# Performance work log

Measured on AMD Instinct MI355X. Metric: run time of the kernel, lower is better.

The kernel has to match this reference:

```python
import jax, jax.numpy as jnp
from jax import lax
import numpy as np

NBINS = 50

def _make_filters():
    coords = np.linspace(-1.0, 1.0, 3)
    zz, yy, xx = np.meshgrid(coords, coords, coords, indexing='ij')
    gf = []
    for freq in [2.0, 4.0]:
        for ang in [0.0, np.pi / 4, np.pi / 2, 3 * np.pi / 4]:
            gauss = np.exp(-(xx ** 2 + yy ** 2 + zz ** 2) / 0.5)
            f = gauss * np.cos(freq * (xx * np.cos(ang) + yy * np.sin(ang)))
            f = f - f.mean()
            s = f.std(ddof=1)  # torch std is unbiased
            if s > 1e-8:
                f = f / s
            gf.append(f)
    gf = np.stack(gf)[:, None].astype(np.float32)  # (8,1,3,3,3)
    lf = []
    for axis in range(3):
        for sign in [1, -1]:
            f = np.zeros((3, 3, 3), np.float32)
            f[1, 1, 1] = 1.0
            idx = [1, 1, 1]
            idx[axis] += sign
            f[tuple(idx)] = -1.0
            lf.append(f)
    lf = np.stack(lf)[:, None].astype(np.float32)  # (6,1,3,3,3)
    return gf, lf

def setup_inputs() -> dict:
    key = jax.random.key(0)
    k1, k2 = jax.random.split(key)
    B, D, H, W = 4, 96, 160, 160
    x = jax.random.uniform(k1, (B, 1, D, H, W), jnp.float32, minval=-1.0, maxval=1.0)
    mask = (jax.random.uniform(k2, (B, 1, D, H, W), jnp.float32) > 0.5).astype(jnp.float32)
    gf, lf = _make_filters()
    return {"x": x, "mask": mask, "gabor_filters": jnp.asarray(gf), "lbp_filters": jnp.asarray(lf)}

def _hu_stats(v, mf):
    # v, mf: (B,D,H,W); mf is 0/1 float mask
    n = mf.sum((1, 2, 3))                      # (B,)
    nn = jnp.maximum(n, 1.0)
    mu = (mf * v).sum((1, 2, 3)) / nn
    diff = (v - mu[:, None, None, None]) * mf
    var = (diff ** 2).sum((1, 2, 3)) / jnp.maximum(n - 1.0, 1.0)  # unbiased, like torch .std()
    sigma = jnp.sqrt(var) + 1e-8
    z = diff / sigma[:, None, None, None]
    skew = (z ** 3).sum((1, 2, 3)) / nn
    kurt = (z ** 4).sum((1, 2, 3)) / nn - 3.0
    # histogram over [-1,1] with 50 bins; torch.histc ignores out-of-range, last bin inclusive
    w = mf * ((v >= -1.0) & (v <= 1.0)).astype(v.dtype)
    idx = jnp.clip(jnp.floor((v + 1.0) * (NBINS / 2.0)).astype(jnp.int32), 0, NBINS - 1)
    hist = jax.vmap(lambda i, wb: jnp.zeros((NBINS,), v.dtype).at[i.ravel()].add(wb.ravel()))(idx, w)
    p = hist / (hist.sum(-1, keepdims=True) + 1e-8)
    ent = -(p * jnp.log(p + 1e-8)).sum(-1)
    valid = (n >= 10.0).astype(v.dtype)
    return jnp.stack([mu, sigma, skew, kurt, ent], axis=1) * valid[:, None]  # (B,5)

def _glcm_proxy(v, m):
    # v: (B,D,H,W) float; m: (B,D,H,W) bool
    rows = []
    for axis in range(3):
        a = axis + 1
        sl1 = tuple(slice(None, -1) if i == a else slice(None) for i in range(4))
        sl2 = tuple(slice(1, None) if i == a else slice(None) for i in range(4))
        d = v[sl1] - v[sl2]
        mp = (m[sl1] & m[sl2]).astype(v.dtype)
        s = mp.sum((1, 2, 3))
        ss = jnp.maximum(s, 1.0)
        con = (mp * d * d).sum((1, 2, 3)) / ss
        hom = (mp / (1.0 + d * d)).sum((1, 2, 3)) / ss
        ok = (s >= 4.0).astype(v.dtype)
        rows += [con * ok, hom * ok]
    return jnp.stack(rows, axis=1)  # (B,6)

def _forward(x, mask, gabor_filters, lbp_filters):
    v = x[:, 0]                       # (B,D,H,W)
    m = mask[:, 0] > 0.5              # bool
    mf = m.astype(x.dtype)
    hu = _hu_stats(v, mf)             # (B,5)
    dn = ('NCDHW', 'OIDHW', 'NCDHW')
    pad = [(1, 1)] * 3
    gab = lax.conv_general_dilated(x, gabor_filters, (1, 1, 1), pad, dimension_numbers=dn)
    lung_vol = jnp.clip(mask.sum((2, 3, 4)), 1.0, None)      # (B,1)
    gab_feat = jnp.abs(gab * mask).sum((2, 3, 4)) / lung_vol  # (B,8)
    lbp = lax.conv_general_dilated(x, lbp_filters, (1, 1, 1), pad, dimension_numbers=dn)
    lbp = lbp * mask
    lbp_feat = ((lbp > 0).astype(x.dtype) * mask).sum((2, 3, 4)) / lung_vol  # (B,6)
    glcm = _glcm_proxy(v, m)          # (B,6)
    return jnp.concatenate([hu, gab_feat, lbp_feat, glcm], axis=1)  # (B,25)

def reference(x, mask, gabor_filters, lbp_filters):
    return _forward(x, mask, gabor_filters, lbp_filters)
```

## Files before the change

kernel.cpp:

```cpp
#include <hip/hip_runtime.h>
#include <math.h>

#define B_    4
#define D_    96
#define H_    160
#define W_    160
#define HW_   (H_ * W_)
#define NVOX  (D_ * H_ * W_)
#define NBINS 50
#define CZ    8
#define NCHUNK (D_ / CZ)
#define NTILE 50
#define NSLOTS (NTILE * NCHUNK)
#define NITEMS (B_ * NSLOTS)
#define NQR   28
#define PART_F (B_ * NQR * NSLOTS)
#define HIST_U PART_F
#define WQ_F   (PART_F + 200)
#define CTR_U  (WQ_F + 40)
#define LASTP ((D_ - 1) * HW_)

typedef float f2 __attribute__((ext_vector_type(2)));

__device__ __forceinline__ float rfl(float v) {
    return __uint_as_float(__builtin_amdgcn_readfirstlane(__float_as_uint(v)));
}

__global__ __launch_bounds__(64) void radiomics_weights(
    const float* __restrict__ gf, const float* __restrict__ lf,
    float* __restrict__ ws)
{
    const int lane = threadIdx.x;
    __shared__ float sCs[8][5], sR[8], sMO[8], sMC[8];
    if (lane < 8) {
        const int f = lane;
        float O9[9], C9[9];
        float mC = 0.f, mO = 0.f;
#pragma unroll
        for (int k = 0; k < 9; ++k) {
            O9[k] = gf[f * 27 + k];
            C9[k] = gf[f * 27 + 9 + k];
            mC += C9[k]; mO += O9[k];
        }
        mC *= (1.f / 9.f); mO *= (1.f / 9.f);
        float cov = 0.f, var = 0.f;
#pragma unroll
        for (int k = 0; k < 9; ++k) {
            float c = C9[k] - mC, o = O9[k] - mO;
            cov += c * o; var += c * c;
        }
        sR[f] = cov / var; sMO[f] = mO; sMC[f] = mC;
#pragma unroll
        for (int j = 0; j < 4; ++j) sCs[f][j] = 0.5f * (C9[j] + C9[8 - j]);
        sCs[f][4] = C9[4];
    }
    __syncthreads();
    if (lane == 0) {
        float* wq = ws + WQ_F;
        float gz0 = 0.f;
        for (int f = 0; f < 8; ++f) gz0 += sR[f];
        gz0 *= 0.125f;
        wq[0] = gz0;
        float df[8];
        for (int f = 0; f < 8; ++f) df[f] = sMO[f] - gz0 * sMC[f];
        for (int F = 0; F < 2; ++F) {
            const int f0 = 4 * F, f1 = 4 * F + 1, f2 = 4 * F + 2, f3 = 4 * F + 3;
            float* g = wq + 1 + 11 * F;
            g[0]  = 0.5f * (df[f0] + df[f2]);
            g[1]  = 0.5f * (sCs[f0][0] + sCs[f2][0]);
            g[2]  = 0.5f * (sCs[f0][2] + sCs[f2][2]);
            g[3]  = 0.5f * (sCs[f0][4] + sCs[f2][4]);
            g[4]  = 0.5f * (sCs[f0][1] + sCs[f2][3]);
            g[5]  = 0.5f * (sCs[f0][3] + sCs[f2][1]);
            g[6]  = 0.5f * (df[f1] + df[f3]);
            g[7]  = 0.25f * (sCs[f1][1] + sCs[f1][3]
                           + sCs[f3][1] + sCs[f3][3]);
            g[8]  = 0.5f * (sCs[f1][4] + sCs[f3][4]);
            g[9]  = 0.5f * (sCs[f1][0] + sCs[f3][2]);
            g[10] = 0.5f * (sCs[f1][2] + sCs[f3][0]);
        }
        const int nbidx[6] = {22, 4, 16, 10, 14, 12};
        for (int f = 0; f < 6; ++f) {
            wq[23 + f] = lf[f * 27 + 13];
            wq[29 + f] = lf[f * 27 + nbidx[f]];
        }
        ((unsigned int*)ws)[CTR_U] = 0u;
    }
    unsigned int* gh = (unsigned int*)ws + HIST_U;
    for (int i = lane; i < B_ * NBINS; i += 64) gh[i] = 0u;
}

#define LOADP(s, zo) do {                                                   \
    _Pragma("unroll")                                                       \
    for (int r_ = 0; r_ < 3; ++r_) {                                        \
        Xw[s][r_][0] = xbb[(zo) + rowoff[r_] + xL];                         \
        f2 t_ = *(const f2*)(xbb + (zo) + rowoff[r_] + gx);                 \
        Xw[s][r_][1] = t_.x; Xw[s][r_][2] = t_.y;                           \
        Xw[s][r_][3] = xbb[(zo) + rowoff[r_] + xR];                         \
    }                                                                       \
} while (0)

#define FINISH(s, bzv) do {                                                 \
    const float br0_ = bndRow0 * (bzv), br2_ = bndRow2 * (bzv);             \
    _Pragma("unroll")                                                       \
    for (int c_ = 0; c_ < 4; ++c_) {                                        \
        Xw[s][0][c_] *= br0_; Xw[s][2][c_] *= br2_; Xw[s][1][c_] *= (bzv);  \
    }                                                                       \
    _Pragma("unroll")                                                       \
    for (int r_ = 0; r_ < 3; ++r_) {                                        \
        Xw[s][r_][0] *= bndL; Xw[s][r_][3] *= bndR;                         \
    }                                                                       \
    {                                                                       \
        float cs0_ = Xw[s][0][0] + Xw[s][1][0] + Xw[s][2][0];               \
        float cs1_ = Xw[s][0][1] + Xw[s][1][1] + Xw[s][2][1];               \
        float cs2_ = Xw[s][0][2] + Xw[s][1][2] + Xw[s][2][2];               \
        float cs3_ = Xw[s][0][3] + Xw[s][1][3] + Xw[s][2][3];               \
        S9[s][0] = cs0_ + cs1_ + cs2_;                                      \
        S9[s][1] = cs1_ + cs2_ + cs3_;                                      \
    }                                                                       \
} while (0)

__global__ __launch_bounds__(256) void radiomics_main(
    const float* __restrict__ x, const float* __restrict__ mask,
    float* __restrict__ ws)
{
    __shared__ unsigned int shist[4 * NBINS];
    __shared__ float xred[4][NQR];
    __shared__ unsigned int sitem;

    const int tid = threadIdx.x;
    const int tx = tid & 15, ty = tid >> 4;
    const int lane = tid & 63, wid = tid >> 6;

    const float* wq = ws + WQ_F;
    const float gz0 = rfl(wq[0]);
    float gco[22];
#pragma unroll
    for (int i = 0; i < 22; ++i) gco[i] = rfl(wq[1 + i]);
    float lwc[6], lwn[6];
#pragma unroll
    for (int f = 0; f < 6; ++f) { lwc[f] = rfl(wq[23 + f]); lwn[f] = rfl(wq[29 + f]); }

    unsigned int* ctr   = (unsigned int*)ws + CTR_U;
    unsigned int* ghist = (unsigned int*)ws + HIST_U;

    for (;;) {
        __syncthreads();
        if (tid == 0) sitem = atomicAdd(ctr, 1u);
        for (int i = tid; i < 4 * NBINS; i += 256) shist[i] = 0u;
        __syncthreads();
        const int item = __builtin_amdgcn_readfirstlane((int)sitem);
        if (item >= NITEMS) break;

        const int b   = item / NSLOTS;
        const int s   = item - b * NSLOTS;
        const int cz  = s / NTILE;
        const int bix = s - cz * NTILE;
        const int z0  = cz * CZ;
        const int gx = (bix % 5) * 32 + tx * 2;
        const int gy = (bix / 5) * 16 + ty;

        const float* __restrict__ xbb = x    + (size_t)b * NVOX;
        const float* __restrict__ mbb = mask + (size_t)b * NVOX;

        const int gy0 = (gy > 0) ? gy - 1 : 0;
        const int gy2 = (gy + 1 < H_) ? gy + 1 : H_ - 1;
        const int rowoff[3] = { gy0 * W_, gy * W_, gy2 * W_ };
        const float bndRow0 = (gy > 0) ? 1.f : 0.f;
        const float bndRow2 = (gy + 1 < H_) ? 1.f : 0.f;
        const int xL = (gx > 0) ? gx - 1 : 0;
        const int xR = (gx + 2 < W_) ? gx + 2 : W_ - 1;
        const float bndL = (gx > 0) ? 1.f : 0.f;
        const float bndR = (gx + 2 < W_) ? 1.f : 0.f;
        const int moff  = gy * W_ + gx;
        const int myoff = gy2 * W_ + gx;
        const int mxoff = gy * W_ + xR;
        const float bym = bndRow2, bxm = bndR;

        float Xw[4][3][4];
        float S9[4][2];
        float Mq[4][2];
        float bzs[4];
        f2    myq[2];
        float mxq[2];
        float acc[NQR];
#pragma unroll
        for (int q = 0; q < NQR; ++q) acc[q] = 0.f;
        bzs[0] = bzs[1] = bzs[2] = 1.f;

        if (z0 == 0) {
#pragma unroll
            for (int r = 0; r < 3; ++r)
#pragma unroll
                for (int c = 0; c < 4; ++c) Xw[0][r][c] = 0.f;
            S9[0][0] = S9[0][1] = 0.f;
        } else {
            LOADP(0, (z0 - 1) * HW_);
            FINISH(0, 1.f);
        }
        LOADP(1, z0 * HW_);
        FINISH(1, 1.f);
        {
            f2 mm = *(const f2*)(mbb + z0 * HW_ + moff);
            Mq[1][0] = (mm.x > 0.5f) ? 1.f : 0.f;
            Mq[1][1] = (mm.y > 0.5f) ? 1.f : 0.f;
        }
        LOADP(2, (z0 + 1) * HW_);
        {
            f2 mm = *(const f2*)(mbb + (z0 + 1) * HW_ + moff);
            Mq[2][0] = mm.x; Mq[2][1] = mm.y;
        }
        Mq[0][0] = Mq[0][1] = 0.f;
        myq[0] = *(const f2*)(mbb + z0 * HW_ + myoff);
        mxq[0] = mbb[z0 * HW_ + mxoff];

        int zc   = z0 * HW_;
        int zpre = (z0 + 2) * HW_;

#pragma unroll 1
        for (int i0 = 0; i0 < CZ; i0 += 4) {
#pragma unroll
            for (int j = 0; j < 4; ++j) {
                const int c0 = j, c1 = (j + 1) & 3, c2 = (j + 2) & 3, c3 = (j + 3) & 3;
                const int cur = j & 1, nxt = cur ^ 1;

                const int zpe = (zpre < NVOX) ? zpre : LASTP;
                bzs[c3] = (zpre < NVOX) ? 1.f : 0.f;
                LOADP(c3, zpe);
                {
                    f2 mm = *(const f2*)(mbb + zpe + moff);
                    Mq[c3][0] = mm.x; Mq[c3][1] = mm.y;
                }
                const int zn = (zc + HW_ < NVOX) ? zc + HW_ : LASTP;
                myq[nxt] = *(const f2*)(mbb + zn + myoff);
                mxq[nxt] = mbb[zn + mxoff];

                FINISH(c2, bzs[c2]);
                Mq[c2][0] = (Mq[c2][0] * bzs[c2] > 0.5f) ? 1.f : 0.f;
                Mq[c2][1] = (Mq[c2][1] * bzs[c2] > 0.5f) ? 1.f : 0.f;

                float T6[3][4];
#pragma unroll
                for (int r = 0; r < 3; ++r)
#pragma unroll
                    for (int c = 0; c < 4; ++c)
                        T6[r][c] = fmaf(gz0, Xw[c0][r][c] + Xw[c2][r][c], Xw[c1][r][c]);

                const f2 my2 = myq[cur];
                const float mxs = mxq[cur];

#pragma unroll
                for (int q = 0; q < 2; ++q) {
                    const float v  = Xw[c1][1][q + 1];
                    const float mc = Mq[c1][q];

                    acc[0] += mc;
                    float mv  = mc * v;  acc[1] += mv;
                    float mv2 = mv * v;  acc[2] += mv2;
                    float mv3 = mv2 * v; acc[3] += mv3;
                    acc[4] += mv3 * v;

                    if (mc > 0.5f && v >= -1.f && v <= 1.f) {
                        int bi = (int)floorf((v + 1.f) * (NBINS * 0.5f));
                        bi = min(max(bi, 0), NBINS - 1);
                        atomicAdd(&shist[(tid >> 6) * NBINS + bi], 1u);
                    }

                    float P0 = T6[0][q]     + T6[2][q + 2];
                    float P1 = T6[0][q + 1] + T6[2][q + 1];
                    float P2 = T6[0][q + 2] + T6[2][q];
                    float P3 = T6[1][q]     + T6[1][q + 2];
                    float ctrv = T6[1][q + 1];
                    float S2 = S9[c0][q] + S9[c2][q];
                    float Qv = P1 + P3;
#pragma unroll
                    for (int F = 0; F < 2; ++F) {
                        const float dfA = gco[F*11+0], c0s = gco[F*11+1];
                        const float c2s = gco[F*11+2], c4s = gco[F*11+3];
                        const float cu  = gco[F*11+4], cw  = gco[F*11+5];
                        const float dfB = gco[F*11+6], ct  = gco[F*11+7];
                        const float ce  = gco[F*11+8], ca  = gco[F*11+9];
                        const float cb  = gco[F*11+10];
                        float E = dfA * S2;
                        E = fmaf(c0s, P0, E); E = fmaf(c2s, P2, E); E = fmaf(c4s, ctrv, E);
                        float r0   = fmaf(cu, P1, fmaf(cw, P3, E));
                        float r90  = fmaf(cw, P1, fmaf(cu, P3, E));
                        float G = fmaf(ct, Qv, dfB * S2);
                        G = fmaf(ce, ctrv, G);
                        float r45  = fmaf(ca, P0, fmaf(cb, P2, G));
                        float r135 = fmaf(cb, P0, fmaf(ca, P2, G));
                        acc[5 + 4*F + 0] = fmaf(fabsf(r0),   mc, acc[5 + 4*F + 0]);
                        acc[5 + 4*F + 1] = fmaf(fabsf(r45),  mc, acc[5 + 4*F + 1]);
                        acc[5 + 4*F + 2] = fmaf(fabsf(r90),  mc, acc[5 + 4*F + 2]);
                        acc[5 + 4*F + 3] = fmaf(fabsf(r135), mc, acc[5 + 4*F + 3]);
                    }

                    const float nb[6] = { Xw[c2][1][q + 1], Xw[c0][1][q + 1],
                                          Xw[c1][2][q + 1], Xw[c1][0][q + 1],
                                          Xw[c1][1][q + 2], Xw[c1][1][q] };
#pragma unroll
                    for (int f = 0; f < 6; ++f) {
                        float l = fmaf(lwc[f], v, lwn[f] * nb[f]);
                        acc[13 + f] += (l > 0.f) ? mc : 0.f;
                    }

                    {
                        float mp = mc * Mq[c2][q];
                        float d = v - Xw[c2][1][q + 1], dd = d * d;
                        acc[19] += mp;
                        acc[22] = fmaf(mp, dd, acc[22]);
                        acc[25] = fmaf(mp, __builtin_amdgcn_rcpf(1.f + dd), acc[25]);
                    }
                    {
                        float mr = (q == 0) ? my2.x : my2.y;
                        float mp = mc * (((mr > 0.5f) ? 1.f : 0.f) * bym);
                        float d = v - Xw[c1][2][q + 1], dd = d * d;
                        acc[20] += mp;
                        acc[23] = fmaf(mp, dd, acc[23]);
                        acc[26] = fmaf(mp, __builtin_amdgcn_rcpf(1.f + dd), acc[26]);
                    }
                    {
                        float mnr = (q == 0) ? Mq[c1][1] : (((mxs > 0.5f) ? 1.f : 0.f) * bxm);
                        float mp = mc * mnr;
                        float d = v - Xw[c1][1][q + 2], dd = d * d;
                        acc[21] += mp;
                        acc[24] = fmaf(mp, dd, acc[24]);
                        acc[27] = fmaf(mp, __builtin_amdgcn_rcpf(1.f + dd), acc[27]);
                    }
                }
                zc += HW_; zpre += HW_;
            }
        }

#pragma unroll
        for (int q = 0; q < NQR; ++q) {
            float sm = acc[q];
#pragma unroll
            for (int o = 32; o > 0; o >>= 1)
                sm += __shfl_down(sm, o, 64);
            acc[q] = sm;
        }
        if (lane == 0) {
#pragma unroll
            for (int q = 0; q < NQR; ++q) xred[wid][q] = acc[q];
        }
        __syncthreads();

        if (tid < NQR) {
            float v = xred[0][tid] + xred[1][tid] + xred[2][tid] + xred[3][tid];
            ws[((size_t)b * NQR + tid) * NSLOTS + s] = v;
        } else if (tid < NQR + NBINS) {
            int h = tid - NQR;
            unsigned int c = shist[h] + shist[NBINS + h]
                           + shist[2 * NBINS + h] + shist[3 * NBINS + h];
            if (c) atomicAdd(&ghist[b * NBINS + h], c);
        }
    }
}

__global__ __launch_bounds__(512) void radiomics_tail(
    const float* __restrict__ ws, float* __restrict__ out)
{
    __shared__ double fin[NQR];
    __shared__ double hcnt[NBINS];
    __shared__ double entp[NBINS];
    __shared__ double sh_hsum;
    const int b = blockIdx.x, tid = threadIdx.x;
    const int wave = tid >> 6, lane = tid & 63;

    for (int q = wave; q < NQR; q += 8) {
        const float* p = ws + ((size_t)b * NQR + q) * NSLOTS;
        double s = 0.0;
#pragma unroll
        for (int k = 0; k < 10; ++k) {
            int idx = lane + 64 * k;
            if (idx < NSLOTS) s += (double)p[idx];
        }
#pragma unroll
        for (int o = 32; o > 0; o >>= 1)
            s += __shfl_down(s, o, 64);
        if (lane == 0) fin[q] = s;
    }
    if (tid < NBINS)
        hcnt[tid] = (double)(((const unsigned int*)ws)[HIST_U + b * NBINS + tid]);
    __syncthreads();

    if (tid == 0) {
        double h = 0.0;
        for (int k = 0; k < NBINS; ++k) h += hcnt[k];
        sh_hsum = h + 1e-8;
    }
    __syncthreads();

    if (tid < NBINS) {
        double p = hcnt[tid] / sh_hsum;
        entp[tid] = -p * log(p + 1e-8);
    }
    __syncthreads();

    if (tid == 0) {
        const double n  = fin[0];
        const double nn = fmax(n, 1.0);
        const double s1 = fin[1], s2 = fin[2], s3 = fin[3], s4 = fin[4];
        const double mu = s1 / nn;
        const double M2 = s2 - 2.0 * mu * s1 + mu * mu * n;
        const double M3 = s3 - 3.0 * mu * s2 + 3.0 * mu * mu * s1 - mu * mu * mu * n;
        const double M4 = s4 - 4.0 * mu * s3 + 6.0 * mu * mu * s2
                          - 4.0 * mu * mu * mu * s1 + mu * mu * mu * mu * n;
        const double var   = M2 / fmax(n - 1.0, 1.0);
        const double sigma = sqrt(var) + 1e-8;
        const double skew  = M3 / (sigma * sigma * sigma) / nn;
        const double kurt  = M4 / (sigma * sigma * sigma * sigma) / nn - 3.0;

        double ent = 0.0;
        for (int k = 0; k < NBINS; ++k) ent += entp[k];

        const double valid = (n >= 10.0) ? 1.0 : 0.0;
        float* ob = out + b * 25;
        ob[0] = (float)(mu * valid);
        ob[1] = (float)(sigma * valid);
        ob[2] = (float)(skew * valid);
        ob[3] = (float)(kurt * valid);
        ob[4] = (float)(ent * valid);

        const double lung = fmax(n, 1.0);
        for (int f = 0; f < 8; ++f) ob[5 + f]  = (float)(fin[5 + f] / lung);
        for (int f = 0; f < 6; ++f) ob[13 + f] = (float)(fin[13 + f] / lung);

        for (int ax = 0; ax < 3; ++ax) {
            double s  = fin[19 + ax];
            double ss = fmax(s, 1.0);
            double ok = (s >= 4.0) ? 1.0 : 0.0;
            ob[19 + 2 * ax]     = (float)(fin[22 + ax] / ss * ok);
            ob[19 + 2 * ax + 1] = (float)(fin[25 + ax] / ss * ok);
        }
    }
}

extern "C" void kernel_launch(void* const* d_in, const int* in_sizes, int n_in,
                              void* d_out, int out_size, void* d_ws, size_t ws_size,
                              hipStream_t stream)
{
    const float* x    = (const float*)d_in[0];
    const float* mask = (const float*)d_in[1];
    const float* gf   = (const float*)d_in[2];
    const float* lf   = (const float*)d_in[3];
    float* out = (float*)d_out;
    float* ws  = (float*)d_ws;

    radiomics_weights<<<1, 64, 0, stream>>>(gf, lf, ws);
    radiomics_main<<<dim3(1024), 256, 0, stream>>>(x, mask, ws);
    radiomics_tail<<<B_, 512, 0, stream>>>(ws, out);
}
```

Before: 185.5 us.

## Replace atomic work queue with static grid of uneven z-chunks per tile

Removes the persistent-block atomic work counter and launches a fixed grid of 256 blocks per batch, each handling one xy tile over a z-chunk of 16 or 20 slices. The chunks are longer than before, so there are fewer halo reloads and fewer reduction and partial-sum writes. The split is uneven, with the first tiles using 6 chunks of 16 and the rest using 5 chunks of 16 or 20, so that the block count lands on 256 per batch. FINISH now branches on the z-boundary flag instead of multiplying by it. In exchange the schedule is static, and blocks with 20 slices take longer than those with 16, which can leave some load imbalance with no dynamic scheduling to absorb it.

```diff
diff --git a/kernel.cpp b/kernel.cpp
--- a/kernel.cpp
+++ b/kernel.cpp
@@ -8,16 +8,11 @@
 #define HW_   (H_ * W_)
 #define NVOX  (D_ * H_ * W_)
 #define NBINS 50
-#define CZ    8
-#define NCHUNK (D_ / CZ)
-#define NTILE 50
-#define NSLOTS (NTILE * NCHUNK)
-#define NITEMS (B_ * NSLOTS)
 #define NQR   28
-#define PART_F (B_ * NQR * NSLOTS)
+#define CPB   256
+#define PART_F (B_ * NQR * CPB)
 #define HIST_U PART_F
 #define WQ_F   (PART_F + 200)
-#define CTR_U  (WQ_F + 40)
 #define LASTP ((D_ - 1) * HW_)
 
 typedef float f2 __attribute__((ext_vector_type(2)));
@@ -84,7 +79,6 @@
             wq[23 + f] = lf[f * 27 + 13];
             wq[29 + f] = lf[f * 27 + nbidx[f]];
         }
-        ((unsigned int*)ws)[CTR_U] = 0u;
     }
     unsigned int* gh = (unsigned int*)ws + HIST_U;
     for (int i = lane; i < B_ * NBINS; i += 64) gh[i] = 0u;
@@ -101,16 +95,21 @@
 } while (0)
 
 #define FINISH(s, bzv) do {                                                 \
-    const float br0_ = bndRow0 * (bzv), br2_ = bndRow2 * (bzv);             \
-    _Pragma("unroll")                                                       \
-    for (int c_ = 0; c_ < 4; ++c_) {                                        \
-        Xw[s][0][c_] *= br0_; Xw[s][2][c_] *= br2_; Xw[s][1][c_] *= (bzv);  \
-    }                                                                       \
-    _Pragma("unroll")                                                       \
-    for (int r_ = 0; r_ < 3; ++r_) {                                        \
-        Xw[s][r_][0] *= bndL; Xw[s][r_][3] *= bndR;                         \
-    }                                                                       \
-    {                                                                       \
+    if ((bzv) == 0.f) {                                                     \
+        _Pragma("unroll")                                                   \
+        for (int r_ = 0; r_ < 3; ++r_)                                      \
+            _Pragma("unroll")                                               \
+            for (int c_ = 0; c_ < 4; ++c_) Xw[s][r_][c_] = 0.f;             \
+        S9[s][0] = S9[s][1] = 0.f;                                          \
+    } else {                                                                \
+        _Pragma("unroll")                                                   \
+        for (int c_ = 0; c_ < 4; ++c_) {                                    \
+            Xw[s][0][c_] *= bndRow0; Xw[s][2][c_] *= bndRow2;               \
+        }                                                                   \
+        _Pragma("unroll")                                                   \
+        for (int r_ = 0; r_ < 3; ++r_) {                                    \
+            Xw[s][r_][0] *= bndL; Xw[s][r_][3] *= bndR;                     \
+        }                                                                   \
         float cs0_ = Xw[s][0][0] + Xw[s][1][0] + Xw[s][2][0];               \
         float cs1_ = Xw[s][0][1] + Xw[s][1][1] + Xw[s][2][1];               \
         float cs2_ = Xw[s][0][2] + Xw[s][1][2] + Xw[s][2][2];               \
@@ -126,12 +125,13 @@
 {
     __shared__ unsigned int shist[4 * NBINS];
     __shared__ float xred[4][NQR];
-    __shared__ unsigned int sitem;
 
     const int tid = threadIdx.x;
     const int tx = tid & 15, ty = tid >> 4;
     const int lane = tid & 63, wid = tid >> 6;
 
+    for (int i = tid; i < 4 * NBINS; i += 256) shist[i] = 0u;
+
     const float* wq = ws + WQ_F;
     const float gz0 = rfl(wq[0]);
     float gco[22];
@@ -141,220 +141,221 @@
 #pragma unroll
     for (int f = 0; f < 6; ++f) { lwc[f] = rfl(wq[23 + f]); lwn[f] = rfl(wq[29 + f]); }
 
-    unsigned int* ctr   = (unsigned int*)ws + CTR_U;
-    unsigned int* ghist = (unsigned int*)ws + HIST_U;
-
-    for (;;) {
-        __syncthreads();
-        if (tid == 0) sitem = atomicAdd(ctr, 1u);
-        for (int i = tid; i < 4 * NBINS; i += 256) shist[i] = 0u;
-        __syncthreads();
-        const int item = __builtin_amdgcn_readfirstlane((int)sitem);
-        if (item >= NITEMS) break;
-
-        const int b   = item / NSLOTS;
-        const int s   = item - b * NSLOTS;
-        const int cz  = s / NTILE;
-        const int bix = s - cz * NTILE;
-        const int z0  = cz * CZ;
-        const int gx = (bix % 5) * 32 + tx * 2;
-        const int gy = (bix / 5) * 16 + ty;
-
-        const float* __restrict__ xbb = x    + (size_t)b * NVOX;
-        const float* __restrict__ mbb = mask + (size_t)b * NVOX;
-
-        const int gy0 = (gy > 0) ? gy - 1 : 0;
-        const int gy2 = (gy + 1 < H_) ? gy + 1 : H_ - 1;
-        const int rowoff[3] = { gy0 * W_, gy * W_, gy2 * W_ };
-        const float bndRow0 = (gy > 0) ? 1.f : 0.f;
-        const float bndRow2 = (gy + 1 < H_) ? 1.f : 0.f;
-        const int xL = (gx > 0) ? gx - 1 : 0;
-        const int xR = (gx + 2 < W_) ? gx + 2 : W_ - 1;
-        const float bndL = (gx > 0) ? 1.f : 0.f;
-        const float bndR = (gx + 2 < W_) ? 1.f : 0.f;
-        const int moff  = gy * W_ + gx;
-        const int myoff = gy2 * W_ + gx;
-        const int mxoff = gy * W_ + xR;
-        const float bym = bndRow2, bxm = bndR;
-
-        float Xw[4][3][4];
-        float S9[4][2];
-        float Mq[4][2];
-        float bzs[4];
-        f2    myq[2];
-        float mxq[2];
-        float acc[NQR];
-#pragma unroll
-        for (int q = 0; q < NQR; ++q) acc[q] = 0.f;
-        bzs[0] = bzs[1] = bzs[2] = 1.f;
-
-        if (z0 == 0) {
+    const int c = blockIdx.x;
+    const int b = blockIdx.z;
+    int t, z0, nz;
+    if (c < 36) {
+        t  = c / 6;
+        const int ci = c - 6 * t;
+        z0 = 16 * ci; nz = 16;
+    } else {
+        const int c2 = c - 36;
+        const int ti = c2 / 5;
+        const int ci = c2 - 5 * ti;
+        t = 6 + ti;
+        if (ci == 0) { z0 = 0; nz = 16; }
+        else         { z0 = 20 * ci - 4; nz = 20; }
+    }
+    const int ngroups = nz >> 2;
+
+    const int gx = (t % 5) * 32 + tx * 2;
+    const int gy = (t / 5) * 16 + ty;
+
+    const float* __restrict__ xbb = x    + (size_t)b * NVOX;
+    const float* __restrict__ mbb = mask + (size_t)b * NVOX;
+
+    const int gy0 = (gy > 0) ? gy - 1 : 0;
+    const int gy2 = (gy + 1 < H_) ? gy + 1 : H_ - 1;
+    const int rowoff[3] = { gy0 * W_, gy * W_, gy2 * W_ };
+    const float bndRow0 = (gy > 0) ? 1.f : 0.f;
+    const float bndRow2 = (gy + 1 < H_) ? 1.f : 0.f;
+    const int xL = (gx > 0) ? gx - 1 : 0;
+    const int xR = (gx + 2 < W_) ? gx + 2 : W_ - 1;
+    const float bndL = (gx > 0) ? 1.f : 0.f;
+    const float bndR = (gx + 2 < W_) ? 1.f : 0.f;
+    const int moff  = gy * W_ + gx;
+    const int myoff = gy2 * W_ + gx;
+    const int mxoff = gy * W_ + xR;
+    const float bym = bndRow2, bxm = bndR;
+
+    float Xw[4][3][4];
+    float S9[4][2];
+    float Mq[4][2];
+    float bzs[4];
+    f2    myq[2];
+    float mxq[2];
+    float acc[NQR];
+#pragma unroll
+    for (int q = 0; q < NQR; ++q) acc[q] = 0.f;
+    bzs[0] = bzs[1] = bzs[2] = 1.f;
+
+    if (z0 == 0) {
+#pragma unroll
+        for (int r = 0; r < 3; ++r)
+#pragma unroll
+            for (int cc = 0; cc < 4; ++cc) Xw[0][r][cc] = 0.f;
+        S9[0][0] = S9[0][1] = 0.f;
+    } else {
+        LOADP(0, (z0 - 1) * HW_);
+        FINISH(0, 1.f);
+    }
+    LOADP(1, z0 * HW_);
+    FINISH(1, 1.f);
+    {
+        f2 mm = *(const f2*)(mbb + z0 * HW_ + moff);
+        Mq[1][0] = (mm.x > 0.5f) ? 1.f : 0.f;
+        Mq[1][1] = (mm.y > 0.5f) ? 1.f : 0.f;
+    }
+    LOADP(2, (z0 + 1) * HW_);
+    {
+        f2 mm = *(const f2*)(mbb + (z0 + 1) * HW_ + moff);
+        Mq[2][0] = mm.x; Mq[2][1] = mm.y;
+    }
+    Mq[0][0] = Mq[0][1] = 0.f;
+    myq[0] = *(const f2*)(mbb + z0 * HW_ + myoff);
+    mxq[0] = mbb[z0 * HW_ + mxoff];
+
+    int zc   = z0 * HW_;
+    int zpre = (z0 + 2) * HW_;
+
+#pragma unroll 1
+    for (int g = 0; g < ngroups; ++g) {
+#pragma unroll
+        for (int j = 0; j < 4; ++j) {
+            const int c0 = j, c1 = (j + 1) & 3, c2 = (j + 2) & 3, c3 = (j + 3) & 3;
+            const int cur = j & 1, nxt = cur ^ 1;
+
+            const int zpe = (zpre < NVOX) ? zpre : LASTP;
+            bzs[c3] = (zpre < NVOX) ? 1.f : 0.f;
+            LOADP(c3, zpe);
+            {
+                f2 mm = *(const f2*)(mbb + zpe + moff);
+                Mq[c3][0] = mm.x; Mq[c3][1] = mm.y;
+            }
+            const int zn = (zc + HW_ < NVOX) ? zc + HW_ : LASTP;
+            myq[nxt] = *(const f2*)(mbb + zn + myoff);
+            mxq[nxt] = mbb[zn + mxoff];
+
+            FINISH(c2, bzs[c2]);
+            Mq[c2][0] = (Mq[c2][0] * bzs[c2] > 0.5f) ? 1.f : 0.f;
+            Mq[c2][1] = (Mq[c2][1] * bzs[c2] > 0.5f) ? 1.f : 0.f;
+
+            float T6[3][4];
 #pragma unroll
             for (int r = 0; r < 3; ++r)
 #pragma unroll
-                for (int c = 0; c < 4; ++c) Xw[0][r][c] = 0.f;
-            S9[0][0] = S9[0][1] = 0.f;
-        } else {
-            LOADP(0, (z0 - 1) * HW_);
-            FINISH(0, 1.f);
-        }
-        LOADP(1, z0 * HW_);
-        FINISH(1, 1.f);
-        {
-            f2 mm = *(const f2*)(mbb + z0 * HW_ + moff);
-            Mq[1][0] = (mm.x > 0.5f) ? 1.f : 0.f;
-            Mq[1][1] = (mm.y > 0.5f) ? 1.f : 0.f;
-        }
-        LOADP(2, (z0 + 1) * HW_);
-        {
-            f2 mm = *(const f2*)(mbb + (z0 + 1) * HW_ + moff);
-            Mq[2][0] = mm.x; Mq[2][1] = mm.y;
-        }
-        Mq[0][0] = Mq[0][1] = 0.f;
-        myq[0] = *(const f2*)(mbb + z0 * HW_ + myoff);
-        mxq[0] = mbb[z0 * HW_ + mxoff];
-
-        int zc   = z0 * HW_;
-        int zpre = (z0 + 2) * HW_;
-
-#pragma unroll 1
-        for (int i0 = 0; i0 < CZ; i0 += 4) {
-#pragma unroll
-            for (int j = 0; j < 4; ++j) {
-                const int c0 = j, c1 = (j + 1) & 3, c2 = (j + 2) & 3, c3 = (j + 3) & 3;
-                const int cur = j & 1, nxt = cur ^ 1;
-
-                const int zpe = (zpre < NVOX) ? zpre : LASTP;
-                bzs[c3] = (zpre < NVOX) ? 1.f : 0.f;
-                LOADP(c3, zpe);
+                for (int cc = 0; cc < 4; ++cc)
+                    T6[r][cc] = fmaf(gz0, Xw[c0][r][cc] + Xw[c2][r][cc], Xw[c1][r][cc]);
+
+            const f2 my2 = myq[cur];
+            const float mxs = mxq[cur];
+
+#pragma unroll
+            for (int q = 0; q < 2; ++q) {
+                const float v  = Xw[c1][1][q + 1];
+                const float mc = Mq[c1][q];
+
+                acc[0] += mc;
+                float mv  = mc * v;  acc[1] += mv;
+                float mv2 = mv * v;  acc[2] += mv2;
+                float mv3 = mv2 * v; acc[3] += mv3;
+                acc[4] += mv3 * v;
+
+                if (mc > 0.5f && v >= -1.f && v <= 1.f) {
+                    int bi = (int)floorf((v + 1.f) * (NBINS * 0.5f));
+                    bi = min(max(bi, 0), NBINS - 1);
+                    atomicAdd(&shist[(tid >> 6) * NBINS + bi], 1u);
+                }
+
+                float P0 = T6[0][q]     + T6[2][q + 2];
+                float P1 = T6[0][q + 1] + T6[2][q + 1];
+                float P2 = T6[0][q + 2] + T6[2][q];
+                float P3 = T6[1][q]     + T6[1][q + 2];
+                float ctrv = T6[1][q + 1];
+                float S2 = S9[c0][q] + S9[c2][q];
+                float Qv = P1 + P3;
+#pragma unroll
+                for (int F = 0; F < 2; ++F) {
+                    const float dfA = gco[F*11+0], c0s = gco[F*11+1];
+                    const float c2s = gco[F*11+2], c4s = gco[F*11+3];
+                    const float cu  = gco[F*11+4], cw  = gco[F*11+5];
+                    const float dfB = gco[F*11+6], ct  = gco[F*11+7];
+                    const float ce  = gco[F*11+8], ca  = gco[F*11+9];
+                    const float cb  = gco[F*11+10];
+                    float E = dfA * S2;
+                    E = fmaf(c0s, P0, E); E = fmaf(c2s, P2, E); E = fmaf(c4s, ctrv, E);
+                    float r0   = fmaf(cu, P1, fmaf(cw, P3, E));
+                    float r90  = fmaf(cw, P1, fmaf(cu, P3, E));
+                    float G = fmaf(ct, Qv, dfB * S2);
+                    G = fmaf(ce, ctrv, G);
+                    float r45  = fmaf(ca, P0, fmaf(cb, P2, G));
+                    float r135 = fmaf(cb, P0, fmaf(ca, P2, G));
+                    acc[5 + 4*F + 0] = fmaf(fabsf(r0),   mc, acc[5 + 4*F + 0]);
+                    acc[5 + 4*F + 1] = fmaf(fabsf(r45),  mc, acc[5 + 4*F + 1]);
+                    acc[5 + 4*F + 2] = fmaf(fabsf(r90),  mc, acc[5 + 4*F + 2]);
+                    acc[5 + 4*F + 3] = fmaf(fabsf(r135), mc, acc[5 + 4*F + 3]);
+                }
+
+                const float nb[6] = { Xw[c2][1][q + 1], Xw[c0][1][q + 1],
+                                      Xw[c1][2][q + 1], Xw[c1][0][q + 1],
+                                      Xw[c1][1][q + 2], Xw[c1][1][q] };
+#pragma unroll
+                for (int f = 0; f < 6; ++f) {
+                    float l = fmaf(lwc[f], v, lwn[f] * nb[f]);
+                    acc[13 + f] += (l > 0.f) ? mc : 0.f;
+                }
+
                 {
-                    f2 mm = *(const f2*)(mbb + zpe + moff);
-                    Mq[c3][0] = mm.x; Mq[c3][1] = mm.y;
-                }
-                const int zn = (zc + HW_ < NVOX) ? zc + HW_ : LASTP;
-                myq[nxt] = *(const f2*)(mbb + zn + myoff);
-                mxq[nxt] = mbb[zn + mxoff];
-
-                FINISH(c2, bzs[c2]);
-                Mq[c2][0] = (Mq[c2][0] * bzs[c2] > 0.5f) ? 1.f : 0.f;
-                Mq[c2][1] = (Mq[c2][1] * bzs[c2] > 0.5f) ? 1.f : 0.f;
-
-                float T6[3][4];
-#pragma unroll
-                for (int r = 0; r < 3; ++r)
-#pragma unroll
-                    for (int c = 0; c < 4; ++c)
-                        T6[r][c] = fmaf(gz0, Xw[c0][r][c] + Xw[c2][r][c], Xw[c1][r][c]);
-
-                const f2 my2 = myq[cur];
-                const float mxs = mxq[cur];
-
-#pragma unroll
-                for (int q = 0; q < 2; ++q) {
-                    const float v  = Xw[c1][1][q + 1];
-                    const float mc = Mq[c1][q];
-
-                    acc[0] += mc;
-                    float mv  = mc * v;  acc[1] += mv;
-                    float mv2 = mv * v;  acc[2] += mv2;
-                    float mv3 = mv2 * v; acc[3] += mv3;
-                    acc[4] += mv3 * v;
-
-                    if (mc > 0.5f && v >= -1.f && v <= 1.f) {
-                        int bi = (int)floorf((v + 1.f) * (NBINS * 0.5f));
-                        bi = min(max(bi, 0), NBINS - 1);
-                        atomicAdd(&shist[(tid >> 6) * NBINS + bi], 1u);
-                    }
-
-                    float P0 = T6[0][q]     + T6[2][q + 2];
-                    float P1 = T6[0][q + 1] + T6[2][q + 1];
-                    float P2 = T6[0][q + 2] + T6[2][q];
-                    float P3 = T6[1][q]     + T6[1][q + 2];
-                    float ctrv = T6[1][q + 1];
-                    float S2 = S9[c0][q] + S9[c2][q];
-                    float Qv = P1 + P3;
-#pragma unroll
-                    for (int F = 0; F < 2; ++F) {
-                        const float dfA = gco[F*11+0], c0s = gco[F*11+1];
-                        const float c2s = gco[F*11+2], c4s = gco[F*11+3];
-                        const float cu  = gco[F*11+4], cw  = gco[F*11+5];
-                        const float dfB = gco[F*11+6], ct  = gco[F*11+7];
-                        const float ce  = gco[F*11+8], ca  = gco[F*11+9];
-                        const float cb  = gco[F*11+10];
-                        float E = dfA * S2;
-                        E = fmaf(c0s, P0, E); E = fmaf(c2s, P2, E); E = fmaf(c4s, ctrv, E);
-                        float r0   = fmaf(cu, P1, fmaf(cw, P3, E));
-                        float r90  = fmaf(cw, P1, fmaf(cu, P3, E));
-                        float G = fmaf(ct, Qv, dfB * S2);
-                        G = fmaf(ce, ctrv, G);
-                        float r45  = fmaf(ca, P0, fmaf(cb, P2, G));
-                        float r135 = fmaf(cb, P0, fmaf(ca, P2, G));
-                        acc[5 + 4*F + 0] = fmaf(fabsf(r0),   mc, acc[5 + 4*F + 0]);
-                        acc[5 + 4*F + 1] = fmaf(fabsf(r45),  mc, acc[5 + 4*F + 1]);
-                        acc[5 + 4*F + 2] = fmaf(fabsf(r90),  mc, acc[5 + 4*F + 2]);
-                        acc[5 + 4*F + 3] = fmaf(fabsf(r135), mc, acc[5 + 4*F + 3]);
-                    }
-
-                    const float nb[6] = { Xw[c2][1][q + 1], Xw[c0][1][q + 1],
-                                          Xw[c1][2][q + 1], Xw[c1][0][q + 1],
-                                          Xw[c1][1][q + 2], Xw[c1][1][q] };
-#pragma unroll
-                    for (int f = 0; f < 6; ++f) {
-                        float l = fmaf(lwc[f], v, lwn[f] * nb[f]);
-                        acc[13 + f] += (l > 0.f) ? mc : 0.f;
-                    }
-
-                    {
-                        float mp = mc * Mq[c2][q];
-                        float d = v - Xw[c2][1][q + 1], dd = d * d;
-                        acc[19] += mp;
-                        acc[22] = fmaf(mp, dd, acc[22]);
-                        acc[25] = fmaf(mp, __builtin_amdgcn_rcpf(1.f + dd), acc[25]);
-                    }
-                    {
-                        float mr = (q == 0) ? my2.x : my2.y;
-                        float mp = mc * (((mr > 0.5f) ? 1.f : 0.f) * bym);
-                        float d = v - Xw[c1][2][q + 1], dd = d * d;
-                        acc[20] += mp;
-                        acc[23] = fmaf(mp, dd, acc[23]);
-                        acc[26] = fmaf(mp, __builtin_amdgcn_rcpf(1.f + dd), acc[26]);
-                    }
-                    {
-                        float mnr = (q == 0) ? Mq[c1][1] : (((mxs > 0.5f) ? 1.f : 0.f) * bxm);
-                        float mp = mc * mnr;
-                        float d = v - Xw[c1][1][q + 2], dd = d * d;
-                        acc[21] += mp;
-                        acc[24] = fmaf(mp, dd, acc[24]);
-                        acc[27] = fmaf(mp, __builtin_amdgcn_rcpf(1.f + dd), acc[27]);
-                    }
-                }
-                zc += HW_; zpre += HW_;
+                    float mp = mc * Mq[c2][q];
+                    float d = v - Xw[c2][1][q + 1], dd = d * d;
+                    acc[19] += mp;
+                    acc[22] = fmaf(mp, dd, acc[22]);
+                    acc[25] = fmaf(mp, __builtin_amdgcn_rcpf(1.f + dd), acc[25]);
+                }
+                {
+                    float mr = (q == 0) ? my2.x : my2.y;
+                    float mp = mc * (((mr > 0.5f) ? 1.f : 0.f) * bym);
+                    float d = v - Xw[c1][2][q + 1], dd = d * d;
+                    acc[20] += mp;
+                    acc[23] = fmaf(mp, dd, acc[23]);
+                    acc[26] = fmaf(mp, __builtin_amdgcn_rcpf(1.f + dd), acc[26]);
+                }
+                {
+                    float mnr = (q == 0) ? Mq[c1][1] : (((mxs > 0.5f) ? 1.f : 0.f) * bxm);
+                    float mp = mc * mnr;
+                    float d = v - Xw[c1][1][q + 2], dd = d * d;
+                    acc[21] += mp;
+                    acc[24] = fmaf(mp, dd, acc[24]);
+                    acc[27] = fmaf(mp, __builtin_amdgcn_rcpf(1.f + dd), acc[27]);
+                }
             }
-        }
-
-#pragma unroll
-        for (int q = 0; q < NQR; ++q) {
-            float sm = acc[q];
-#pragma unroll
-            for (int o = 32; o > 0; o >>= 1)
-                sm += __shfl_down(sm, o, 64);
-            acc[q] = sm;
-        }
-        if (lane == 0) {
-#pragma unroll
-            for (int q = 0; q < NQR; ++q) xred[wid][q] = acc[q];
-        }
-        __syncthreads();
-
-        if (tid < NQR) {
-            float v = xred[0][tid] + xred[1][tid] + xred[2][tid] + xred[3][tid];
-            ws[((size_t)b * NQR + tid) * NSLOTS + s] = v;
-        } else if (tid < NQR + NBINS) {
-            int h = tid - NQR;
-            unsigned int c = shist[h] + shist[NBINS + h]
-                           + shist[2 * NBINS + h] + shist[3 * NBINS + h];
-            if (c) atomicAdd(&ghist[b * NBINS + h], c);
-        }
+            zc += HW_; zpre += HW_;
+        }
+    }
+
+#pragma unroll
+    for (int q = 0; q < NQR; ++q) {
+        float sm = acc[q];
+#pragma unroll
+        for (int o = 32; o > 0; o >>= 1)
+            sm += __shfl_down(sm, o, 64);
+        acc[q] = sm;
+    }
+    if (lane == 0) {
+#pragma unroll
+        for (int q = 0; q < NQR; ++q) xred[wid][q] = acc[q];
+    }
+    __syncthreads();
+
+    if (tid < NQR) {
+        float v = xred[0][tid] + xred[1][tid] + xred[2][tid] + xred[3][tid];
+        ws[((size_t)b * NQR + tid) * CPB + c] = v;
+    } else if (tid < NQR + NBINS) {
+        int h = tid - NQR;
+        unsigned int cnt = shist[h] + shist[NBINS + h]
+                         + shist[2 * NBINS + h] + shist[3 * NBINS + h];
+        unsigned int* ghist = (unsigned int*)ws + HIST_U;
+        if (cnt) atomicAdd(&ghist[b * NBINS + h], cnt);
     }
 }
 
@@ -369,13 +370,11 @@
     const int wave = tid >> 6, lane = tid & 63;
 
     for (int q = wave; q < NQR; q += 8) {
-        const float* p = ws + ((size_t)b * NQR + q) * NSLOTS;
+        const float* p = ws + ((size_t)b * NQR + q) * CPB;
         double s = 0.0;
 #pragma unroll
-        for (int k = 0; k < 10; ++k) {
-            int idx = lane + 64 * k;
-            if (idx < NSLOTS) s += (double)p[idx];
-        }
+        for (int k = 0; k < 4; ++k)
+            s += (double)p[lane + 64 * k];
 #pragma unroll
         for (int o = 32; o > 0; o >>= 1)
             s += __shfl_down(s, o, 64);
@@ -449,6 +448,6 @@
     float* ws  = (float*)d_ws;
 
     radiomics_weights<<<1, 64, 0, stream>>>(gf, lf, ws);
-    radiomics_main<<<dim3(1024), 256, 0, stream>>>(x, mask, ws);
+    radiomics_main<<<dim3(256, 1, B_), 256, 0, stream>>>(x, mask, ws);
     radiomics_tail<<<B_, 512, 0, stream>>>(ws, out);
 }
```

Result: faster. 166.1 us (-10.5%).
